# Kernel optimization log

Hardware: AMD Instinct MI355X
Metric: run time of the kernel (lower is better)

The kernel has to match this reference:

```python
import jax, jax.numpy as jnp
import numpy as np

C = 128          # multiplicity of 0e and 1o irreps
N = 16384        # number of tokens / points
SQRT2 = 2.0 ** 0.5
SQRT3 = 3.0 ** 0.5


def _tensor_square(s, v):
    """Per-channel symmetric tensor square of (1x0e + 1x1o).
    s: (N,C) scalars, v: (N,C,3) vectors.
    Returns ss:(N,C) 0e, sv:(N,C,3) 1o, vv0:(N,C) 0e, q:(N,C,5) 2e."""
    ss = s * s
    sv = SQRT2 * s[..., None] * v
    vv0 = jnp.sum(v * v, axis=-1) / SQRT3
    x, y, z = v[..., 0], v[..., 1], v[..., 2]
    q = jnp.stack([
        SQRT3 * x * y,
        SQRT3 * y * z,
        (2.0 * z * z - x * x - y * y) / 2.0,
        SQRT3 * x * z,
        SQRT3 * (x * x - y * y) / 2.0,
    ], axis=-1)
    return ss, sv, vv0, q


def _block(s, v, w1, w2, w0, wv):
    """_SelfInteractionBlock: tensor_square + concat/regroup + invariant-gated MLP + equivariant Linear."""
    ss, sv, vv0, q = _tensor_square(s, v)
    # regrouped features: 3C x 0e, 2C x 1o, C x 2e
    sc = jnp.concatenate([s, ss, vv0], axis=-1)            # (N, 3C)
    vec = jnp.concatenate([v, sv], axis=1)                 # (N, 2C, 3)
    # gate MLP on invariants (fan-in normalized, silu hidden)
    h = jax.nn.silu(sc @ w1 / jnp.sqrt(jnp.float32(sc.shape[-1])))
    g = h @ w2 / jnp.sqrt(jnp.float32(h.shape[-1]))        # (N, 6C) one gate per irrep
    g_s = g[:, :3 * C]
    g_v = g[:, 3 * C:5 * C]
    # (2e gates multiply q, which is dropped by the Linear to Cx0e+Cx1o)
    sc = sc * g_s
    vec = vec * g_v[..., None]
    # block-diagonal equivariant Linear -> C x 0e + C x 1o
    out_s = sc @ w0 / jnp.sqrt(jnp.float32(sc.shape[-1]))                      # (N, C)
    out_v = jnp.einsum('nmd,mc->ncd', vec, wv) / jnp.sqrt(jnp.float32(vec.shape[1]))  # (N, C, 3)
    return out_s, out_v


def _eq_layernorm(s, v, g0, g1, eps=1e-6):
    mu = jnp.mean(s, axis=-1, keepdims=True)
    sd = jnp.sqrt(jnp.mean((s - mu) ** 2, axis=-1, keepdims=True) + eps)
    s = (s - mu) / sd * g0
    rms = jnp.sqrt(jnp.mean(v * v, axis=(1, 2), keepdims=True) + eps)
    v = v / rms * g1[None, :, None]
    return s, v


def setup_inputs() -> dict:
    key = jax.random.key(0)
    ks = jax.random.split(key, 6)
    x = jax.random.normal(ks[0], (N, 4 * C), dtype=jnp.float32)
    mlp_w1 = jax.random.normal(ks[1], (2, 3 * C, 3 * C), dtype=jnp.float32)
    mlp_w2 = jax.random.normal(ks[2], (2, 3 * C, 6 * C), dtype=jnp.float32)
    lin_w0 = jax.random.normal(ks[3], (2, 3 * C, C), dtype=jnp.float32)
    lin_w1 = jax.random.normal(ks[4], (2, 2 * C, C), dtype=jnp.float32)
    ln_g0 = jnp.ones((C,), dtype=jnp.float32)
    ln_g1 = jnp.ones((C,), dtype=jnp.float32)
    return {"x": x, "mlp_w1": mlp_w1, "mlp_w2": mlp_w2,
            "lin_w0": lin_w0, "lin_w1": lin_w1, "ln_g0": ln_g0, "ln_g1": ln_g1}


def reference(x, mlp_w1, mlp_w2, lin_w0, lin_w1, ln_g0, ln_g1):
    n = x.shape[0]
    s = x[:, :C]                         # C x 0e
    v = x[:, C:].reshape(n, C, 3)        # C x 1o
    n_layers = mlp_w1.shape[0]
    for i in range(n_layers):
        ds, dv = _block(s, v, mlp_w1[i], mlp_w2[i], lin_w0[i], lin_w1[i])
        s = s + ds   # residual
        v = v + dv
        if i != n_layers - 1:  # norm on all but last layer (norm_last=False)
            s, v = _eq_layernorm(s, v, ln_g0, ln_g1)
    return jnp.concatenate([s, v.reshape(n, 3 * C)], axis=-1)
```

## Files before the change

kernel.cpp:

```cpp
#include <hip/hip_runtime.h>


typedef _Float16 half8 __attribute__((ext_vector_type(8)));
typedef float floatx4 __attribute__((ext_vector_type(4)));

static inline int cdiv_h(int a, int b){ return (a + b - 1) / b; }


__device__ __forceinline__ void stage16(const char* gaddr, char* lds_base){
  __builtin_amdgcn_global_load_lds((const __attribute__((address_space(1))) unsigned int*)gaddr,
                                   (__attribute__((address_space(3))) unsigned int*)lds_base,
                                   16, 0, 0);
}

__device__ __forceinline__ float wave_sum64(float x){
  #pragma unroll
  for (int m = 32; m; m >>= 1) x += __shfl_xor(x, m, 64);
  return x;
}

__device__ __forceinline__ void split_store(_Float16* p0, _Float16* p1, float v){
  _Float16 hi = (_Float16)v;
  *p0 = hi;
  *p1 = (_Float16)(v - (float)hi);
}

__device__ __forceinline__ unsigned int pack_split(float v){
  union { _Float16 h[2]; unsigned int u; } pk;
  _Float16 hi = (_Float16)v;
  pk.h[0] = hi;
  pk.h[1] = (_Float16)(v - (float)hi);
  return pk.u;
}

__device__ __forceinline__ void unzip16(uint4 p, uint2& hi, uint2& lo){
  hi.x = (p.x & 0xffffu) | (p.y << 16);
  hi.y = (p.z & 0xffffu) | (p.w << 16);
  lo.x = (p.x >> 16) | (p.y & 0xffff0000u);
  lo.y = (p.z >> 16) | (p.w & 0xffff0000u);
}

__device__ __forceinline__ void remap_xcd(int id, int nx, int ny, int& x, int& y){
  if (ny & 7){ x = id % nx; y = id / nx; return; }
  int xcd = id & 7, q = id >> 3, t = q / nx;
  x = q - t*nx; y = xcd + (t << 3);
}

__global__ __launch_bounds__(256) void prep_all(const float* __restrict__ w1,
                                                const float* __restrict__ w2,
                                                const float* __restrict__ w0,
                                                const float* __restrict__ wv,
                                                _Float16* __restrict__ W){
  const int PER_L = 475136;
  int idx = blockIdx.x*256 + threadIdx.x;
  if (idx >= 2*PER_L) return;
  int l = idx / PER_L;
  int r = idx - l*PER_L;
  const float RS384 = 0.051031036307982884f;
  _Float16* WL = W + (size_t)l*1425408;
  const float* src; _Float16* dst; int K, ldw, col, k; float scale;
  if (r < 147456){
    src = w1 + (size_t)l*147456; dst = WL;            K = 384; ldw = 384; scale = RS384;
    col = r / 384; k = r - col*384;
  } else if (r < 393216){
    r -= 147456;
    src = w2 + (size_t)l*294912; dst = WL + 442368;   K = 384; ldw = 768; scale = RS384;
    col = r / 384; k = r - col*384;
  } else if (r < 442368){
    r -= 393216;
    src = w0 + (size_t)l*49152;  dst = WL + 1179648;  K = 384; ldw = 128; scale = RS384;
    col = r / 384; k = r - col*384;
  } else {
    r -= 442368;
    src = wv + (size_t)l*32768;  dst = WL + 1327104;  K = 256; ldw = 128; scale = 0.0625f;
    col = r / 256; k = r - col*256;
  }
  float v = src[(size_t)k*ldw + col] * scale;
  _Float16 hi = (_Float16)v;
  _Float16 lo = (_Float16)(v - (float)hi);
  size_t b = (size_t)col*3*K + k;
  dst[b]       = hi;
  dst[b + K]   = lo;
  dst[b + 2*K] = hi;
}

__global__ __launch_bounds__(256) void e0_fused(const float* __restrict__ x,
                                                float* __restrict__ S,
                                                float* __restrict__ V,
                                                _Float16* __restrict__ A1,
                                                int row0){
  __shared__ alignas(16) float lx[4][512];
  const int n0 = blockIdx.x*4;
  const int tid = threadIdx.x;
  const float4* xs = (const float4*)(x + (size_t)(row0 + n0)*512);
  float4* ls = (float4*)(&lx[0][0]);
  ls[tid]       = xs[tid];
  ls[tid + 256] = xs[tid + 256];
  __syncthreads();
  const int w = tid >> 6, lane = tid & 63;
  const int n = n0 + w;
  const float* row = &lx[w][0];
  #pragma unroll
  for (int h = 0; h < 2; ++h){
    int ch = h*64 + lane;
    float s = row[ch];
    S[(size_t)n*128 + ch] = s;
    float vv = 0.f;
    #pragma unroll
    for (int d = 0; d < 3; ++d){
      float vd = row[128 + ch*3 + d];
      V[((size_t)n*3 + d)*128 + ch] = vd;
      vv += vd*vd;
    }
    float vals[3] = { s, s*s, vv * 0.5773502691896258f };
    #pragma unroll
    for (int q = 0; q < 3; ++q){
      size_t b = (size_t)n*768 + q*128 + ch;
      split_store(&A1[b], &A1[b + 384], vals[q]);
    }
  }
}

__global__ __launch_bounds__(256) void e3_fin(float* __restrict__ S, float* __restrict__ V,
                                              const float* __restrict__ OS, const float* __restrict__ OV,
                                              const float* __restrict__ g0, const float* __restrict__ g1,
                                              float* __restrict__ out, _Float16* __restrict__ A1,
                                              int row0, int doln){
  int n = blockIdx.x*4 + (threadIdx.x >> 6);
  int lane = threadIdx.x & 63;
  size_t sb = (size_t)n*128;
  size_t vb = (size_t)n*384;
  float s0 = S[sb + lane]      + OS[sb + lane];
  float s1 = S[sb + 64 + lane] + OS[sb + 64 + lane];
  float v[6];
  #pragma unroll
  for (int k = 0; k < 6; ++k) v[k] = V[vb + k*64 + lane] + OV[vb + k*64 + lane];

  if (doln){
    float mu = wave_sum64(s0 + s1) * (1.0f/128.0f);
    float d0 = s0 - mu, d1 = s1 - mu;
    float var = wave_sum64(d0*d0 + d1*d1) * (1.0f/128.0f);
    float sd = sqrtf(var + 1e-6f);
    float vvsum = 0.f;
    #pragma unroll
    for (int k = 0; k < 6; ++k) vvsum += v[k]*v[k];
    float rms = sqrtf(wave_sum64(vvsum) * (1.0f/384.0f) + 1e-6f);
    float s0n = d0 / sd * g0[lane];
    float s1n = d1 / sd * g0[64 + lane];
    S[sb + lane]      = s0n;
    S[sb + 64 + lane] = s1n;
    float vn[6];
    #pragma unroll
    for (int k = 0; k < 6; ++k){
      int j = k*64 + lane;
      vn[k] = v[k] / rms * g1[j & 127];
      V[vb + j] = vn[k];
    }
    float vv_a = vn[0]*vn[0] + vn[2]*vn[2] + vn[4]*vn[4];
    float vv_b = vn[1]*vn[1] + vn[3]*vn[3] + vn[5]*vn[5];
    float va[3] = { s0n, s0n*s0n, vv_a * 0.5773502691896258f };
    float vbv[3]= { s1n, s1n*s1n, vv_b * 0.5773502691896258f };
    #pragma unroll
    for (int q = 0; q < 3; ++q){
      size_t ba = (size_t)n*768 + q*128 + lane;
      split_store(&A1[ba], &A1[ba + 384], va[q]);
      size_t bb = ba + 64;
      split_store(&A1[bb], &A1[bb + 384], vbv[q]);
    }
  } else {
    size_t ob = (size_t)(row0 + n)*512;
    out[ob + lane]      = s0;
    out[ob + 64 + lane] = s1;
    #pragma unroll
    for (int k = 0; k < 6; ++k){
      int j = k*64 + lane;
      int d = j >> 7, ch = j & 127;
      out[ob + 128 + ch*3 + d] = v[k];
    }
  }
}

__device__ __forceinline__ void gemm_mainloop(const _Float16* __restrict__ A,
                                              const _Float16* __restrict__ BT,
                                              int lda, int kbase, int m0, int c0,
                                              _Float16 (&lsA)[2][4096],
                                              _Float16 (&lsB)[2][2048],
                                              floatx4 (&acc)[4][2]){
  const int nsc  = kbase >> 5;
  const int nch  = 3*nsc;
  const int ldbt = 3*kbase;
  const int tid  = threadIdx.x;
  const int wave = tid >> 6, lane = tid & 63;
  const int wm = wave & 1, wn = wave >> 1;
  const int r = lane & 15, kg = lane >> 4;
  const int slot = kg ^ ((r >> 1) & 3);

  auto stage = [&](int c, int buf){
    const int ka = ((c < nsc) ? c : c - nsc) << 5;
    const int kb = c << 5;
    #pragma unroll
    for (int p = 0; p < 2; ++p){
      const int lbase = wave*1024 + p*4096;
      const int off = lbase + lane*16;
      const int row = off >> 6;
      const int bir = (off & 63) ^ (((off >> 7) & 3) << 4);
      const char* ga = (const char*)A + (((size_t)(m0 + row))*lda + ka)*2 + bir;
      stage16(ga, (char*)(&lsA[buf][0]) + lbase);
    }
    {
      const int lbase = wave*1024;
      const int off = lbase + lane*16;
      const int row = off >> 6;
      const int bir = (off & 63) ^ (((off >> 7) & 3) << 4);
      const char* gb = (const char*)BT + (((size_t)(c0 + row))*ldbt + kb)*2 + bir;
      stage16(gb, (char*)(&lsB[buf][0]) + lbase);
    }
  };

  stage(0, 0);
  for (int c = 0; c < nch; ++c){
    __syncthreads();
    if (c + 1 < nch) stage(c + 1, (c + 1) & 1);
    const char* a_ = (const char*)&lsA[c & 1][0];
    const char* b_ = (const char*)&lsB[c & 1][0];
    half8 af[4], bf[2];
    #pragma unroll
    for (int mt = 0; mt < 4; ++mt)
      af[mt] = *(const half8*)(a_ + ((wm*64 + mt*16 + r)*64 + slot*16));
    #pragma unroll
    for (int nt = 0; nt < 2; ++nt)
      bf[nt] = *(const half8*)(b_ + ((wn*32 + nt*16 + r)*64 + slot*16));
    #pragma unroll
    for (int mt = 0; mt < 4; ++mt)
      #pragma unroll
      for (int nt = 0; nt < 2; ++nt)
        acc[mt][nt] = __builtin_amdgcn_mfma_f32_16x16x32_f16(af[mt], bf[nt], acc[mt][nt], 0, 0, 0);
  }
}

template<int MODE>
__global__ __launch_bounds__(256, 4) void gemm_split(const _Float16* __restrict__ A,
                                                     const _Float16* __restrict__ BT,
                                                     _Float16* __restrict__ OUT,
                                                     const float* __restrict__ S,
                                                     const float* __restrict__ V,
                                                     _Float16* __restrict__ A1g,
                                                     _Float16* __restrict__ A4,
                                                     int lda, int kbase, int nx, int ny){
  __shared__ alignas(16) _Float16 lsA[2][4096];
  __shared__ alignas(16) _Float16 lsB[2][2048];
  int bx, by; remap_xcd(blockIdx.x, nx, ny, bx, by);
  const int c0 = bx << 6, m0 = by << 7;
  floatx4 acc[4][2];
  #pragma unroll
  for (int i = 0; i < 4; ++i)
    #pragma unroll
    for (int j = 0; j < 2; ++j) acc[i][j] = (floatx4){0.f, 0.f, 0.f, 0.f};

  gemm_mainloop(A, BT, lda, kbase, m0, c0, lsA, lsB, acc);

  const int tid = threadIdx.x;
  const int wave = tid >> 6, lane = tid & 63;
  const int wm = wave & 1, wn = wave >> 1;
  const int r = lane & 15, kg = lane >> 4;
  char* scr = (char*)&lsA[0][0];

  if (MODE == 1){
    #pragma unroll
    for (int h = 0; h < 2; ++h){
      __syncthreads();
      if (wm == h){
        #pragma unroll
        for (int mt = 0; mt < 4; ++mt)
          #pragma unroll
          for (int nt = 0; nt < 2; ++nt)
            #pragma unroll
            for (int i = 0; i < 4; ++i){
              int rl = mt*16 + kg*4 + i;
              int cl = wn*32 + nt*16 + r;
              int pc = cl ^ (kg << 4);
              float g = acc[mt][nt][i];
              float hh = g / (1.0f + __expf(-g));
              *(unsigned int*)(scr + rl*256 + pc*4) = pack_split(hh);
            }
      }
      __syncthreads();
      #pragma unroll 1
      for (int j = 0; j < 4; ++j){
        int lin = j*256 + tid, rl = lin >> 4, seg = lin & 15;
        int cs = seg ^ (((rl >> 2) & 3) << 2);
        uint4 p = *(const uint4*)(scr + rl*256 + cs*16);
        uint2 hi, lo; unzip16(p, hi, lo);
        _Float16* rowp = OUT + (size_t)(m0 + h*64 + rl)*768 + c0 + seg*4;
        *(uint2*)rowp         = hi;
        *(uint2*)(rowp + 384) = lo;
      }
    }
  } else if (c0 < 384){
    #pragma unroll
    for (int h = 0; h < 2; ++h){
      __syncthreads();
      #pragma unroll 1
      for (int j = 0; j < 2; ++j){
        int lin = j*256 + tid, rl = lin >> 3, seg = lin & 7;
        int cs = seg ^ (((rl >> 2) & 3) << 1);
        const _Float16* gp = A1g + (size_t)(m0 + h*64 + rl)*768 + c0 + seg*8;
        *(float4*)(scr + rl*128 + cs*16)        = *(const float4*)gp;
        *(float4*)(scr + 8192 + rl*128 + cs*16) = *(const float4*)(gp + 384);
      }
      __syncthreads();
      if (wm == h){
        #pragma unroll
        for (int mt = 0; mt < 4; ++mt)
          #pragma unroll
          for (int nt = 0; nt < 2; ++nt)
            #pragma unroll
            for (int i = 0; i < 4; ++i){
              int rl = mt*16 + kg*4 + i;
              int cl = wn*32 + nt*16 + r;
              int pc = cl ^ (kg << 4);
              _Float16* phi = (_Float16*)scr + rl*64 + pc;
              _Float16* plo = (_Float16*)(scr + 8192) + rl*64 + pc;
              float sc = (float)*phi + (float)*plo;
              split_store(phi, plo, sc * acc[mt][nt][i]);
            }
      }
      __syncthreads();
      #pragma unroll 1
      for (int j = 0; j < 2; ++j){
        int lin = j*256 + tid, rl = lin >> 3, seg = lin & 7;
        int cs = seg ^ (((rl >> 2) & 3) << 1);
        _Float16* gp = A1g + (size_t)(m0 + h*64 + rl)*768 + c0 + seg*8;
        *(float4*)gp         = *(const float4*)(scr + rl*128 + cs*16);
        *(float4*)(gp + 384) = *(const float4*)(scr + 8192 + rl*128 + cs*16);
      }
    }
  } else {
    const int mm0 = c0 - 384;
    const int ch0 = mm0 & 127;
    if (mm0 >= 128){
      #pragma unroll
      for (int mt = 0; mt < 4; ++mt)
        #pragma unroll
        for (int nt = 0; nt < 2; ++nt)
          #pragma unroll
          for (int i = 0; i < 4; ++i){
            int row = m0 + wm*64 + mt*16 + kg*4 + i;
            int cl  = wn*32 + nt*16 + r;
            acc[mt][nt][i] *= 1.4142135623730951f * S[(size_t)row*128 + ch0 + cl];
          }
    }
    for (int d = 0; d < 3; ++d){
      #pragma unroll
      for (int h = 0; h < 2; ++h){
        __syncthreads();
        #pragma unroll 1
        for (int j = 0; j < 4; ++j){
          int lin = j*256 + tid, rl = lin >> 4, seg = lin & 15;
          int cs = seg ^ (((rl >> 2) & 3) << 2);
          *(float4*)(scr + rl*256 + cs*16) =
            *(const float4*)(V + ((size_t)(m0 + h*64 + rl)*3 + d)*128 + ch0 + seg*4);
        }
        __syncthreads();
        if (wm == h){
          #pragma unroll
          for (int mt = 0; mt < 4; ++mt)
            #pragma unroll
            for (int nt = 0; nt < 2; ++nt)
              #pragma unroll
              for (int i = 0; i < 4; ++i){
                int rl = mt*16 + kg*4 + i;
                int cl = wn*32 + nt*16 + r;
                int pc = cl ^ (kg << 4);
                float* pw = (float*)(scr + rl*256) + pc;
                *(unsigned int*)pw = pack_split(*pw * acc[mt][nt][i]);
              }
        }
        __syncthreads();
        #pragma unroll 1
        for (int j = 0; j < 4; ++j){
          int lin = j*256 + tid, rl = lin >> 4, seg = lin & 15;
          int cs = seg ^ (((rl >> 2) & 3) << 2);
          uint4 p = *(const uint4*)(scr + rl*256 + cs*16);
          uint2 hi, lo; unzip16(p, hi, lo);
          _Float16* rowp = A4 + ((size_t)(m0 + h*64 + rl)*3 + d)*512 + mm0 + seg*4;
          *(uint2*)rowp         = hi;
          *(uint2*)(rowp + 256) = lo;
        }
      }
    }
  }
}

__global__ __launch_bounds__(256, 4) void gemm_pair(const _Float16* __restrict__ Aa,
                                                    const _Float16* __restrict__ Ba,
                                                    float* __restrict__ Ca, int ny0,
                                                    const _Float16* __restrict__ Ab,
                                                    const _Float16* __restrict__ Bb,
                                                    float* __restrict__ Cb, int ny1){
  __shared__ alignas(16) _Float16 lsA[2][4096];
  __shared__ alignas(16) _Float16 lsB[2][2048];
  const _Float16 *A, *BT; float* C; int lda, kbase, bx, by;
  const int id = blockIdx.x;
  if (id < 2*ny0){
    remap_xcd(id, 2, ny0, bx, by);
    A = Aa; BT = Ba; C = Ca; lda = 768; kbase = 384;
  } else {
    remap_xcd(id - 2*ny0, 2, ny1, bx, by);
    A = Ab; BT = Bb; C = Cb; lda = 512; kbase = 256;
  }
  const int c0 = bx << 6, m0 = by << 7;
  floatx4 acc[4][2];
  #pragma unroll
  for (int i = 0; i < 4; ++i)
    #pragma unroll
    for (int j = 0; j < 2; ++j) acc[i][j] = (floatx4){0.f, 0.f, 0.f, 0.f};

  gemm_mainloop(A, BT, lda, kbase, m0, c0, lsA, lsB, acc);

  const int wave = threadIdx.x >> 6, lane = threadIdx.x & 63;
  const int wm = wave & 1, wn = wave >> 1;
  const int r = lane & 15, kg = lane >> 4;
  #pragma unroll
  for (int mt = 0; mt < 4; ++mt)
    #pragma unroll
    for (int nt = 0; nt < 2; ++nt)
      #pragma unroll
      for (int i = 0; i < 4; ++i){
        const int row = m0 + wm*64 + mt*16 + kg*4 + i;
        const int col = c0 + wn*32 + nt*16 + r;
        C[(size_t)row*128 + col] = acc[mt][nt][i];
      }
}


extern "C" void kernel_launch(void* const* d_in, const int* in_sizes, int n_in,
                              void* d_out, int out_size, void* d_ws, size_t ws_size,
                              hipStream_t stream){
  const float* x  = (const float*)d_in[0];
  const float* w1 = (const float*)d_in[1];
  const float* w2 = (const float*)d_in[2];
  const float* w0 = (const float*)d_in[3];
  const float* wv = (const float*)d_in[4];
  const float* g0 = (const float*)d_in[5];
  const float* g1 = (const float*)d_in[6];
  float* out = (float*)d_out;
  const int N = in_sizes[0] / 512;

  const size_t HL = 1425408;
  _Float16* W = (_Float16*)d_ws;
  const size_t wbytes = 2*HL*2;

  int cnum = 128;
  for (int cc = 1; cc <= 128; cc <<= 1){
    size_t need = wbytes + (size_t)(N/cc)*10240;
    if (need <= ws_size){ cnum = cc; break; }
  }
  const int R = N / cnum;
  const int ny = R / 128;

  char* p = (char*)d_ws + wbytes;
  float*    Sst = (float*)p;     p += (size_t)R*512;
  float*    Vst = (float*)p;     p += (size_t)R*1536;
  _Float16* A1  = (_Float16*)p;  p += (size_t)R*1536;
  _Float16* A2  = (_Float16*)p;  p += (size_t)R*1536;
  _Float16* A4  = (_Float16*)p;  p += (size_t)R*3072;
  float*    OS  = (float*)p;     p += (size_t)R*512;
  float*    OV  = (float*)p;     p += (size_t)R*1536;

  prep_all<<<cdiv_h(2*475136,256),256,0,stream>>>(w1, w2, w0, wv, W);

  for (int chk = 0; chk < cnum; ++chk){
    const int row0 = chk*R;
    e0_fused<<<R/4,256,0,stream>>>(x, Sst, Vst, A1, row0);
    for (int l = 0; l < 2; ++l){
      _Float16* W1p = W + (size_t)l*HL;
      _Float16* W2p = W1p + 442368;
      _Float16* W0p = W1p + 1179648;
      _Float16* WVp = W1p + 1327104;
      gemm_split<1><<<6*ny,256,0,stream>>>(A1, W1p, A2,
          nullptr, nullptr, nullptr, nullptr, 768, 384, 6, ny);
      gemm_split<2><<<10*ny,256,0,stream>>>(A2, W2p, nullptr,
          Sst, Vst, A1, A4, 768, 384, 10, ny);
      gemm_pair<<<8*ny,256,0,stream>>>(A1, W0p, OS, ny, A4, WVp, OV, 3*ny);
      e3_fin<<<R/4,256,0,stream>>>(Sst, Vst, OS, OV, g0, g1, out, A1, row0, (l == 0) ? 1 : 0);
    }
  }
}
```

Baseline: 390.5 us.

## Deepen GEMM LDS pipeline to four stages with explicit vmcnt waits

The GEMM mainloop goes from a double-buffered LDS ring to a 4-deep ring that prefetches three chunks ahead. Each step uses explicit s_waitcnt vmcnt counts and a raw s_barrier, so the wait covers only the chunk about to be read instead of draining every outstanding load. The larger LDS footprint lets the epilogues stage the full 128-row tile at once, which removes the two-half loop and its extra barriers. The cost is more LDS per block: launch bounds drop to 3 blocks per CU, so occupancy and latency hiding across blocks may fall.

```diff
diff --git a/kernel.cpp b/kernel.cpp
--- a/kernel.cpp
+++ b/kernel.cpp
@@ -183,8 +183,8 @@
 __device__ __forceinline__ void gemm_mainloop(const _Float16* __restrict__ A,
                                               const _Float16* __restrict__ BT,
                                               int lda, int kbase, int m0, int c0,
-                                              _Float16 (&lsA)[2][4096],
-                                              _Float16 (&lsB)[2][2048],
+                                              _Float16 (&lsA)[4][4096],
+                                              _Float16 (&lsB)[4][2048],
                                               floatx4 (&acc)[4][2]){
   const int nsc  = kbase >> 5;
   const int nch  = 3*nsc;
@@ -217,12 +217,18 @@
     }
   };
 
-  stage(0, 0);
+  stage(0, 0); stage(1, 1); stage(2, 2);
   for (int c = 0; c < nch; ++c){
-    __syncthreads();
-    if (c + 1 < nch) stage(c + 1, (c + 1) & 1);
-    const char* a_ = (const char*)&lsA[c & 1][0];
-    const char* b_ = (const char*)&lsB[c & 1][0];
+    const int rem = nch - 1 - c;
+    __builtin_amdgcn_sched_barrier(0);
+    if (rem >= 2)      asm volatile("s_waitcnt vmcnt(6) lgkmcnt(0)" ::: "memory");
+    else if (rem == 1) asm volatile("s_waitcnt vmcnt(3) lgkmcnt(0)" ::: "memory");
+    else               asm volatile("s_waitcnt vmcnt(0) lgkmcnt(0)" ::: "memory");
+    __builtin_amdgcn_s_barrier();
+    __builtin_amdgcn_sched_barrier(0);
+    if (c + 3 < nch) stage(c + 3, (c + 3) & 3);
+    const char* a_ = (const char*)&lsA[c & 3][0];
+    const char* b_ = (const char*)&lsB[c & 3][0];
     half8 af[4], bf[2];
     #pragma unroll
     for (int mt = 0; mt < 4; ++mt)
@@ -239,7 +245,7 @@
 }
 
 template<int MODE>
-__global__ __launch_bounds__(256, 4) void gemm_split(const _Float16* __restrict__ A,
+__global__ __launch_bounds__(256, 3) void gemm_split(const _Float16* __restrict__ A,
                                                      const _Float16* __restrict__ BT,
                                                      _Float16* __restrict__ OUT,
                                                      const float* __restrict__ S,
@@ -247,8 +253,8 @@
                                                      _Float16* __restrict__ A1g,
                                                      _Float16* __restrict__ A4,
                                                      int lda, int kbase, int nx, int ny){
-  __shared__ alignas(16) _Float16 lsA[2][4096];
-  __shared__ alignas(16) _Float16 lsB[2][2048];
+  __shared__ alignas(16) _Float16 lsA[4][4096];
+  __shared__ alignas(16) _Float16 lsB[4][2048];
   int bx, by; remap_xcd(blockIdx.x, nx, ny, bx, by);
   const int c0 = bx << 6, m0 = by << 7;
   floatx4 acc[4][2];
@@ -266,74 +272,64 @@
   char* scr = (char*)&lsA[0][0];
 
   if (MODE == 1){
-    #pragma unroll
-    for (int h = 0; h < 2; ++h){
-      __syncthreads();
-      if (wm == h){
+    __syncthreads();
+    #pragma unroll
+    for (int mt = 0; mt < 4; ++mt)
+      #pragma unroll
+      for (int nt = 0; nt < 2; ++nt)
         #pragma unroll
-        for (int mt = 0; mt < 4; ++mt)
-          #pragma unroll
-          for (int nt = 0; nt < 2; ++nt)
-            #pragma unroll
-            for (int i = 0; i < 4; ++i){
-              int rl = mt*16 + kg*4 + i;
-              int cl = wn*32 + nt*16 + r;
-              int pc = cl ^ (kg << 4);
-              float g = acc[mt][nt][i];
-              float hh = g / (1.0f + __expf(-g));
-              *(unsigned int*)(scr + rl*256 + pc*4) = pack_split(hh);
-            }
-      }
-      __syncthreads();
-      #pragma unroll 1
-      for (int j = 0; j < 4; ++j){
-        int lin = j*256 + tid, rl = lin >> 4, seg = lin & 15;
-        int cs = seg ^ (((rl >> 2) & 3) << 2);
-        uint4 p = *(const uint4*)(scr + rl*256 + cs*16);
-        uint2 hi, lo; unzip16(p, hi, lo);
-        _Float16* rowp = OUT + (size_t)(m0 + h*64 + rl)*768 + c0 + seg*4;
-        *(uint2*)rowp         = hi;
-        *(uint2*)(rowp + 384) = lo;
-      }
+        for (int i = 0; i < 4; ++i){
+          int rl = wm*64 + mt*16 + kg*4 + i;
+          int cl = wn*32 + nt*16 + r;
+          int pc = cl ^ (kg << 4);
+          float g = acc[mt][nt][i];
+          float hh = g / (1.0f + __expf(-g));
+          *(unsigned int*)(scr + rl*256 + pc*4) = pack_split(hh);
+        }
+    __syncthreads();
+    #pragma unroll 1
+    for (int j = 0; j < 8; ++j){
+      int lin = j*256 + tid, rl = lin >> 4, seg = lin & 15;
+      int cs = seg ^ (((rl >> 2) & 3) << 2);
+      uint4 p = *(const uint4*)(scr + rl*256 + cs*16);
+      uint2 hi, lo; unzip16(p, hi, lo);
+      _Float16* rowp = OUT + (size_t)(m0 + rl)*768 + c0 + seg*4;
+      *(uint2*)rowp         = hi;
+      *(uint2*)(rowp + 384) = lo;
     }
   } else if (c0 < 384){
-    #pragma unroll
-    for (int h = 0; h < 2; ++h){
-      __syncthreads();
-      #pragma unroll 1
-      for (int j = 0; j < 2; ++j){
-        int lin = j*256 + tid, rl = lin >> 3, seg = lin & 7;
-        int cs = seg ^ (((rl >> 2) & 3) << 1);
-        const _Float16* gp = A1g + (size_t)(m0 + h*64 + rl)*768 + c0 + seg*8;
-        *(float4*)(scr + rl*128 + cs*16)        = *(const float4*)gp;
-        *(float4*)(scr + 8192 + rl*128 + cs*16) = *(const float4*)(gp + 384);
-      }
-      __syncthreads();
-      if (wm == h){
+    __syncthreads();
+    #pragma unroll 1
+    for (int j = 0; j < 4; ++j){
+      int lin = j*256 + tid, rl = lin >> 3, seg = lin & 7;
+      int cs = seg ^ (((rl >> 2) & 3) << 1);
+      const _Float16* gp = A1g + (size_t)(m0 + rl)*768 + c0 + seg*8;
+      *(float4*)(scr + rl*128 + cs*16)         = *(const float4*)gp;
+      *(float4*)(scr + 16384 + rl*128 + cs*16) = *(const float4*)(gp + 384);
+    }
+    __syncthreads();
+    #pragma unroll
+    for (int mt = 0; mt < 4; ++mt)
+      #pragma unroll
+      for (int nt = 0; nt < 2; ++nt)
         #pragma unroll
-        for (int mt = 0; mt < 4; ++mt)
-          #pragma unroll
-          for (int nt = 0; nt < 2; ++nt)
-            #pragma unroll
-            for (int i = 0; i < 4; ++i){
-              int rl = mt*16 + kg*4 + i;
-              int cl = wn*32 + nt*16 + r;
-              int pc = cl ^ (kg << 4);
-              _Float16* phi = (_Float16*)scr + rl*64 + pc;
-              _Float16* plo = (_Float16*)(scr + 8192) + rl*64 + pc;
-              float sc = (float)*phi + (float)*plo;
-              split_store(phi, plo, sc * acc[mt][nt][i]);
-            }
-      }
-      __syncthreads();
-      #pragma unroll 1
-      for (int j = 0; j < 2; ++j){
-        int lin = j*256 + tid, rl = lin >> 3, seg = lin & 7;
-        int cs = seg ^ (((rl >> 2) & 3) << 1);
-        _Float16* gp = A1g + (size_t)(m0 + h*64 + rl)*768 + c0 + seg*8;
-        *(float4*)gp         = *(const float4*)(scr + rl*128 + cs*16);
-        *(float4*)(gp + 384) = *(const float4*)(scr + 8192 + rl*128 + cs*16);
-      }
+        for (int i = 0; i < 4; ++i){
+          int rl = wm*64 + mt*16 + kg*4 + i;
+          int cl = wn*32 + nt*16 + r;
+          int pc = cl ^ (kg << 4);
+          _Float16* phi = (_Float16*)scr + rl*64 + pc;
+          _Float16* plo = (_Float16*)(scr + 16384) + rl*64 + pc;
+          float sc = (float)*phi + (float)*plo;
+          split_store(phi, plo, sc * acc[mt][nt][i]);
+        }
+    __syncthreads();
+    #pragma unroll 1
+    for (int j = 0; j < 4; ++j){
+      int lin = j*256 + tid, rl = lin >> 3, seg = lin & 7;
+      int cs = seg ^ (((rl >> 2) & 3) << 1);
+      _Float16* gp = A1g + (size_t)(m0 + rl)*768 + c0 + seg*8;
+      *(float4*)gp         = *(const float4*)(scr + rl*128 + cs*16);
+      *(float4*)(gp + 384) = *(const float4*)(scr + 16384 + rl*128 + cs*16);
     }
   } else {
     const int mm0 = c0 - 384;
@@ -351,55 +347,50 @@
           }
     }
     for (int d = 0; d < 3; ++d){
-      #pragma unroll
-      for (int h = 0; h < 2; ++h){
-        __syncthreads();
-        #pragma unroll 1
-        for (int j = 0; j < 4; ++j){
-          int lin = j*256 + tid, rl = lin >> 4, seg = lin & 15;
-          int cs = seg ^ (((rl >> 2) & 3) << 2);
-          *(float4*)(scr + rl*256 + cs*16) =
-            *(const float4*)(V + ((size_t)(m0 + h*64 + rl)*3 + d)*128 + ch0 + seg*4);
-        }
-        __syncthreads();
-        if (wm == h){
+      __syncthreads();
+      #pragma unroll 1
+      for (int j = 0; j < 8; ++j){
+        int lin = j*256 + tid, rl = lin >> 4, seg = lin & 15;
+        int cs = seg ^ (((rl >> 2) & 3) << 2);
+        *(float4*)(scr + rl*256 + cs*16) =
+          *(const float4*)(V + ((size_t)(m0 + rl)*3 + d)*128 + ch0 + seg*4);
+      }
+      __syncthreads();
+      #pragma unroll
+      for (int mt = 0; mt < 4; ++mt)
+        #pragma unroll
+        for (int nt = 0; nt < 2; ++nt)
           #pragma unroll
-          for (int mt = 0; mt < 4; ++mt)
-            #pragma unroll
-            for (int nt = 0; nt < 2; ++nt)
-              #pragma unroll
-              for (int i = 0; i < 4; ++i){
-                int rl = mt*16 + kg*4 + i;
-                int cl = wn*32 + nt*16 + r;
-                int pc = cl ^ (kg << 4);
-                float* pw = (float*)(scr + rl*256) + pc;
-                *(unsigned int*)pw = pack_split(*pw * acc[mt][nt][i]);
-              }
-        }
-        __syncthreads();
-        #pragma unroll 1
-        for (int j = 0; j < 4; ++j){
-          int lin = j*256 + tid, rl = lin >> 4, seg = lin & 15;
-          int cs = seg ^ (((rl >> 2) & 3) << 2);
-          uint4 p = *(const uint4*)(scr + rl*256 + cs*16);
-          uint2 hi, lo; unzip16(p, hi, lo);
-          _Float16* rowp = A4 + ((size_t)(m0 + h*64 + rl)*3 + d)*512 + mm0 + seg*4;
-          *(uint2*)rowp         = hi;
-          *(uint2*)(rowp + 256) = lo;
-        }
+          for (int i = 0; i < 4; ++i){
+            int rl = wm*64 + mt*16 + kg*4 + i;
+            int cl = wn*32 + nt*16 + r;
+            int pc = cl ^ (kg << 4);
+            float* pw = (float*)(scr + rl*256) + pc;
+            *(unsigned int*)pw = pack_split(*pw * acc[mt][nt][i]);
+          }
+      __syncthreads();
+      #pragma unroll 1
+      for (int j = 0; j < 8; ++j){
+        int lin = j*256 + tid, rl = lin >> 4, seg = lin & 15;
+        int cs = seg ^ (((rl >> 2) & 3) << 2);
+        uint4 p = *(const uint4*)(scr + rl*256 + cs*16);
+        uint2 hi, lo; unzip16(p, hi, lo);
+        _Float16* rowp = A4 + ((size_t)(m0 + rl)*3 + d)*512 + mm0 + seg*4;
+        *(uint2*)rowp         = hi;
+        *(uint2*)(rowp + 256) = lo;
       }
     }
   }
 }
 
-__global__ __launch_bounds__(256, 4) void gemm_pair(const _Float16* __restrict__ Aa,
+__global__ __launch_bounds__(256, 3) void gemm_pair(const _Float16* __restrict__ Aa,
                                                     const _Float16* __restrict__ Ba,
                                                     float* __restrict__ Ca, int ny0,
                                                     const _Float16* __restrict__ Ab,
                                                     const _Float16* __restrict__ Bb,
                                                     float* __restrict__ Cb, int ny1){
-  __shared__ alignas(16) _Float16 lsA[2][4096];
-  __shared__ alignas(16) _Float16 lsB[2][2048];
+  __shared__ alignas(16) _Float16 lsA[4][4096];
+  __shared__ alignas(16) _Float16 lsB[4][2048];
   const _Float16 *A, *BT; float* C; int lda, kbase, bx, by;
   const int id = blockIdx.x;
   if (id < 2*ny0){
```

Result: slower. 412.3 us (+5.6%).

## Widen GEMM block tiles from 128x64 to 128x128 across all split GEMMs

Applied to the files above, without the earlier changes.

Doubles the N-dimension of each GEMM workgroup tile to 128 columns, so each wave computes a 64x64 sub-tile with 16 MFMA accumulators instead of 8. A and B now share one LDS buffer, and all epilogues (silu gating, scalar/vector gating, the A4 scatter) are re-indexed for the wider tile. Grids are halved, which cuts redundant A-tile loads and raises MFMA work per LDS read. The cost is more accumulator registers, which may hurt occupancy under launch_bounds(256,4), and fewer workgroups to fill the GPU.

```diff
diff --git a/kernel.cpp b/kernel.cpp
--- a/kernel.cpp
+++ b/kernel.cpp
@@ -183,9 +183,8 @@
 __device__ __forceinline__ void gemm_mainloop(const _Float16* __restrict__ A,
                                               const _Float16* __restrict__ BT,
                                               int lda, int kbase, int m0, int c0,
-                                              _Float16 (&lsA)[2][4096],
-                                              _Float16 (&lsB)[2][2048],
-                                              floatx4 (&acc)[4][2]){
+                                              _Float16 (&ls)[2][8192],
+                                              floatx4 (&acc)[4][4]){
   const int nsc  = kbase >> 5;
   const int nch  = 3*nsc;
   const int ldbt = 3*kbase;
@@ -205,15 +204,9 @@
       const int row = off >> 6;
       const int bir = (off & 63) ^ (((off >> 7) & 3) << 4);
       const char* ga = (const char*)A + (((size_t)(m0 + row))*lda + ka)*2 + bir;
-      stage16(ga, (char*)(&lsA[buf][0]) + lbase);
-    }
-    {
-      const int lbase = wave*1024;
-      const int off = lbase + lane*16;
-      const int row = off >> 6;
-      const int bir = (off & 63) ^ (((off >> 7) & 3) << 4);
+      stage16(ga, (char*)(&ls[buf][0]) + lbase);
       const char* gb = (const char*)BT + (((size_t)(c0 + row))*ldbt + kb)*2 + bir;
-      stage16(gb, (char*)(&lsB[buf][0]) + lbase);
+      stage16(gb, (char*)(&ls[buf][4096]) + lbase);
     }
   };
 
@@ -221,19 +214,19 @@
   for (int c = 0; c < nch; ++c){
     __syncthreads();
     if (c + 1 < nch) stage(c + 1, (c + 1) & 1);
-    const char* a_ = (const char*)&lsA[c & 1][0];
-    const char* b_ = (const char*)&lsB[c & 1][0];
-    half8 af[4], bf[2];
+    const char* a_ = (const char*)&ls[c & 1][0];
+    const char* b_ = (const char*)&ls[c & 1][4096];
+    half8 af[4], bf[4];
     #pragma unroll
     for (int mt = 0; mt < 4; ++mt)
       af[mt] = *(const half8*)(a_ + ((wm*64 + mt*16 + r)*64 + slot*16));
     #pragma unroll
-    for (int nt = 0; nt < 2; ++nt)
-      bf[nt] = *(const half8*)(b_ + ((wn*32 + nt*16 + r)*64 + slot*16));
+    for (int nt = 0; nt < 4; ++nt)
+      bf[nt] = *(const half8*)(b_ + ((wn*64 + nt*16 + r)*64 + slot*16));
     #pragma unroll
     for (int mt = 0; mt < 4; ++mt)
       #pragma unroll
-      for (int nt = 0; nt < 2; ++nt)
+      for (int nt = 0; nt < 4; ++nt)
         acc[mt][nt] = __builtin_amdgcn_mfma_f32_16x16x32_f16(af[mt], bf[nt], acc[mt][nt], 0, 0, 0);
   }
 }
@@ -247,23 +240,22 @@
                                                      _Float16* __restrict__ A1g,
                                                      _Float16* __restrict__ A4,
                                                      int lda, int kbase, int nx, int ny){
-  __shared__ alignas(16) _Float16 lsA[2][4096];
-  __shared__ alignas(16) _Float16 lsB[2][2048];
+  __shared__ alignas(16) _Float16 ls[2][8192];
   int bx, by; remap_xcd(blockIdx.x, nx, ny, bx, by);
-  const int c0 = bx << 6, m0 = by << 7;
-  floatx4 acc[4][2];
+  const int c0 = bx << 7, m0 = by << 7;
+  floatx4 acc[4][4];
   #pragma unroll
   for (int i = 0; i < 4; ++i)
     #pragma unroll
-    for (int j = 0; j < 2; ++j) acc[i][j] = (floatx4){0.f, 0.f, 0.f, 0.f};
-
-  gemm_mainloop(A, BT, lda, kbase, m0, c0, lsA, lsB, acc);
+    for (int j = 0; j < 4; ++j) acc[i][j] = (floatx4){0.f, 0.f, 0.f, 0.f};
+
+  gemm_mainloop(A, BT, lda, kbase, m0, c0, ls, acc);
 
   const int tid = threadIdx.x;
   const int wave = tid >> 6, lane = tid & 63;
   const int wm = wave & 1, wn = wave >> 1;
   const int r = lane & 15, kg = lane >> 4;
-  char* scr = (char*)&lsA[0][0];
+  char* scr = (char*)&ls[0][0];
 
   if (MODE == 1){
     #pragma unroll
@@ -273,81 +265,80 @@
         #pragma unroll
         for (int mt = 0; mt < 4; ++mt)
           #pragma unroll
-          for (int nt = 0; nt < 2; ++nt)
+          for (int nt = 0; nt < 4; ++nt)
             #pragma unroll
             for (int i = 0; i < 4; ++i){
               int rl = mt*16 + kg*4 + i;
-              int cl = wn*32 + nt*16 + r;
+              int cl = wn*64 + nt*16 + r;
               int pc = cl ^ (kg << 4);
               float g = acc[mt][nt][i];
               float hh = g / (1.0f + __expf(-g));
-              *(unsigned int*)(scr + rl*256 + pc*4) = pack_split(hh);
+              *(unsigned int*)(scr + rl*512 + pc*4) = pack_split(hh);
             }
       }
+      __syncthreads();
+      #pragma unroll 1
+      for (int j = 0; j < 8; ++j){
+        int lin = j*256 + tid, rl = lin >> 5, seg = lin & 31;
+        int cs = seg ^ (((rl >> 2) & 3) << 2);
+        uint4 p = *(const uint4*)(scr + rl*512 + cs*16);
+        uint2 hi, lo; unzip16(p, hi, lo);
+        _Float16* rowp = OUT + (size_t)(m0 + h*64 + rl)*768 + c0 + seg*4;
+        *(uint2*)rowp         = hi;
+        *(uint2*)(rowp + 384) = lo;
+      }
+    }
+  } else if (c0 < 384){
+    #pragma unroll
+    for (int h = 0; h < 2; ++h){
       __syncthreads();
       #pragma unroll 1
       for (int j = 0; j < 4; ++j){
         int lin = j*256 + tid, rl = lin >> 4, seg = lin & 15;
-        int cs = seg ^ (((rl >> 2) & 3) << 2);
-        uint4 p = *(const uint4*)(scr + rl*256 + cs*16);
-        uint2 hi, lo; unzip16(p, hi, lo);
-        _Float16* rowp = OUT + (size_t)(m0 + h*64 + rl)*768 + c0 + seg*4;
-        *(uint2*)rowp         = hi;
-        *(uint2*)(rowp + 384) = lo;
-      }
-    }
-  } else if (c0 < 384){
-    #pragma unroll
-    for (int h = 0; h < 2; ++h){
-      __syncthreads();
-      #pragma unroll 1
-      for (int j = 0; j < 2; ++j){
-        int lin = j*256 + tid, rl = lin >> 3, seg = lin & 7;
         int cs = seg ^ (((rl >> 2) & 3) << 1);
         const _Float16* gp = A1g + (size_t)(m0 + h*64 + rl)*768 + c0 + seg*8;
-        *(float4*)(scr + rl*128 + cs*16)        = *(const float4*)gp;
-        *(float4*)(scr + 8192 + rl*128 + cs*16) = *(const float4*)(gp + 384);
+        *(float4*)(scr + rl*256 + cs*16)         = *(const float4*)gp;
+        *(float4*)(scr + 16384 + rl*256 + cs*16) = *(const float4*)(gp + 384);
       }
       __syncthreads();
       if (wm == h){
         #pragma unroll
         for (int mt = 0; mt < 4; ++mt)
           #pragma unroll
-          for (int nt = 0; nt < 2; ++nt)
+          for (int nt = 0; nt < 4; ++nt)
             #pragma unroll
             for (int i = 0; i < 4; ++i){
               int rl = mt*16 + kg*4 + i;
-              int cl = wn*32 + nt*16 + r;
+              int cl = wn*64 + nt*16 + r;
               int pc = cl ^ (kg << 4);
-              _Float16* phi = (_Float16*)scr + rl*64 + pc;
-              _Float16* plo = (_Float16*)(scr + 8192) + rl*64 + pc;
+              _Float16* phi = (_Float16*)scr + rl*128 + pc;
+              _Float16* plo = (_Float16*)(scr + 16384) + rl*128 + pc;
               float sc = (float)*phi + (float)*plo;
               split_store(phi, plo, sc * acc[mt][nt][i]);
             }
       }
       __syncthreads();
       #pragma unroll 1
-      for (int j = 0; j < 2; ++j){
-        int lin = j*256 + tid, rl = lin >> 3, seg = lin & 7;
+      for (int j = 0; j < 4; ++j){
+        int lin = j*256 + tid, rl = lin >> 4, seg = lin & 15;
         int cs = seg ^ (((rl >> 2) & 3) << 1);
         _Float16* gp = A1g + (size_t)(m0 + h*64 + rl)*768 + c0 + seg*8;
-        *(float4*)gp         = *(const float4*)(scr + rl*128 + cs*16);
-        *(float4*)(gp + 384) = *(const float4*)(scr + 8192 + rl*128 + cs*16);
+        *(float4*)gp         = *(const float4*)(scr + rl*256 + cs*16);
+        *(float4*)(gp + 384) = *(const float4*)(scr + 16384 + rl*256 + cs*16);
       }
     }
   } else {
     const int mm0 = c0 - 384;
-    const int ch0 = mm0 & 127;
-    if (mm0 >= 128){
+    if (mm0 == 128){
       #pragma unroll
       for (int mt = 0; mt < 4; ++mt)
         #pragma unroll
-        for (int nt = 0; nt < 2; ++nt)
+        for (int nt = 0; nt < 4; ++nt)
           #pragma unroll
           for (int i = 0; i < 4; ++i){
             int row = m0 + wm*64 + mt*16 + kg*4 + i;
-            int cl  = wn*32 + nt*16 + r;
-            acc[mt][nt][i] *= 1.4142135623730951f * S[(size_t)row*128 + ch0 + cl];
+            int cl  = wn*64 + nt*16 + r;
+            acc[mt][nt][i] *= 1.4142135623730951f * S[(size_t)row*128 + cl];
           }
     }
     for (int d = 0; d < 3; ++d){
@@ -355,33 +346,33 @@
       for (int h = 0; h < 2; ++h){
         __syncthreads();
         #pragma unroll 1
-        for (int j = 0; j < 4; ++j){
-          int lin = j*256 + tid, rl = lin >> 4, seg = lin & 15;
+        for (int j = 0; j < 8; ++j){
+          int lin = j*256 + tid, rl = lin >> 5, seg = lin & 31;
           int cs = seg ^ (((rl >> 2) & 3) << 2);
-          *(float4*)(scr + rl*256 + cs*16) =
-            *(const float4*)(V + ((size_t)(m0 + h*64 + rl)*3 + d)*128 + ch0 + seg*4);
+          *(float4*)(scr + rl*512 + cs*16) =
+            *(const float4*)(V + ((size_t)(m0 + h*64 + rl)*3 + d)*128 + seg*4);
         }
         __syncthreads();
         if (wm == h){
           #pragma unroll
           for (int mt = 0; mt < 4; ++mt)
             #pragma unroll
-            for (int nt = 0; nt < 2; ++nt)
+            for (int nt = 0; nt < 4; ++nt)
               #pragma unroll
               for (int i = 0; i < 4; ++i){
                 int rl = mt*16 + kg*4 + i;
-                int cl = wn*32 + nt*16 + r;
+                int cl = wn*64 + nt*16 + r;
                 int pc = cl ^ (kg << 4);
-                float* pw = (float*)(scr + rl*256) + pc;
+                float* pw = (float*)(scr + rl*512) + pc;
                 *(unsigned int*)pw = pack_split(*pw * acc[mt][nt][i]);
               }
         }
         __syncthreads();
         #pragma unroll 1
-        for (int j = 0; j < 4; ++j){
-          int lin = j*256 + tid, rl = lin >> 4, seg = lin & 15;
+        for (int j = 0; j < 8; ++j){
+          int lin = j*256 + tid, rl = lin >> 5, seg = lin & 31;
           int cs = seg ^ (((rl >> 2) & 3) << 2);
-          uint4 p = *(const uint4*)(scr + rl*256 + cs*16);
+          uint4 p = *(const uint4*)(scr + rl*512 + cs*16);
           uint2 hi, lo; unzip16(p, hi, lo);
           _Float16* rowp = A4 + ((size_t)(m0 + h*64 + rl)*3 + d)*512 + mm0 + seg*4;
           *(uint2*)rowp         = hi;
@@ -398,25 +389,24 @@
                                                     const _Float16* __restrict__ Ab,
                                                     const _Float16* __restrict__ Bb,
                                                     float* __restrict__ Cb, int ny1){
-  __shared__ alignas(16) _Float16 lsA[2][4096];
-  __shared__ alignas(16) _Float16 lsB[2][2048];
+  __shared__ alignas(16) _Float16 ls[2][8192];
   const _Float16 *A, *BT; float* C; int lda, kbase, bx, by;
   const int id = blockIdx.x;
-  if (id < 2*ny0){
-    remap_xcd(id, 2, ny0, bx, by);
+  if (id < ny0){
+    remap_xcd(id, 1, ny0, bx, by);
     A = Aa; BT = Ba; C = Ca; lda = 768; kbase = 384;
   } else {
-    remap_xcd(id - 2*ny0, 2, ny1, bx, by);
+    remap_xcd(id - ny0, 1, ny1, bx, by);
     A = Ab; BT = Bb; C = Cb; lda = 512; kbase = 256;
   }
-  const int c0 = bx << 6, m0 = by << 7;
-  floatx4 acc[4][2];
+  const int m0 = by << 7;
+  floatx4 acc[4][4];
   #pragma unroll
   for (int i = 0; i < 4; ++i)
     #pragma unroll
-    for (int j = 0; j < 2; ++j) acc[i][j] = (floatx4){0.f, 0.f, 0.f, 0.f};
-
-  gemm_mainloop(A, BT, lda, kbase, m0, c0, lsA, lsB, acc);
+    for (int j = 0; j < 4; ++j) acc[i][j] = (floatx4){0.f, 0.f, 0.f, 0.f};
+
+  gemm_mainloop(A, BT, lda, kbase, m0, 0, ls, acc);
 
   const int wave = threadIdx.x >> 6, lane = threadIdx.x & 63;
   const int wm = wave & 1, wn = wave >> 1;
@@ -424,11 +414,11 @@
   #pragma unroll
   for (int mt = 0; mt < 4; ++mt)
     #pragma unroll
-    for (int nt = 0; nt < 2; ++nt)
+    for (int nt = 0; nt < 4; ++nt)
       #pragma unroll
       for (int i = 0; i < 4; ++i){
         const int row = m0 + wm*64 + mt*16 + kg*4 + i;
-        const int col = c0 + wn*32 + nt*16 + r;
+        const int col = wn*64 + nt*16 + r;
         C[(size_t)row*128 + col] = acc[mt][nt][i];
       }
 }
@@ -478,11 +468,11 @@
       _Float16* W2p = W1p + 442368;
       _Float16* W0p = W1p + 1179648;
       _Float16* WVp = W1p + 1327104;
-      gemm_split<1><<<6*ny,256,0,stream>>>(A1, W1p, A2,
-          nullptr, nullptr, nullptr, nullptr, 768, 384, 6, ny);
-      gemm_split<2><<<10*ny,256,0,stream>>>(A2, W2p, nullptr,
-          Sst, Vst, A1, A4, 768, 384, 10, ny);
-      gemm_pair<<<8*ny,256,0,stream>>>(A1, W0p, OS, ny, A4, WVp, OV, 3*ny);
+      gemm_split<1><<<3*ny,256,0,stream>>>(A1, W1p, A2,
+          nullptr, nullptr, nullptr, nullptr, 768, 384, 3, ny);
+      gemm_split<2><<<5*ny,256,0,stream>>>(A2, W2p, nullptr,
+          Sst, Vst, A1, A4, 768, 384, 5, ny);
+      gemm_pair<<<4*ny,256,0,stream>>>(A1, W0p, OS, ny, A4, WVp, OV, 3*ny);
       e3_fin<<<R/4,256,0,stream>>>(Sst, Vst, OS, OV, g0, g1, out, A1, row0, (l == 0) ? 1 : 0);
     }
   }
```

New measurement: 407.8 us. 1.04x slower.

## Stage hi and lo split-fp16 tiles together and issue three MFMAs per chunk

Applied to the files above, without the earlier changes.

The split-fp16 GEMM previously ran the K loop over a tripled K dimension (hi*hi, lo-part, hi-part concatenated), restaging A and B for each third. Now each K chunk loads A-hi, A-lo, B-hi and B-lo into one enlarged LDS buffer and issues the three cross-product MFMA sets from the same registers. This cuts loop iterations, barriers and redundant reloads of the A hi tile. The weight layout drops the duplicated hi copy. The cost is more LDS per block (48KB versus 24KB), so the occupancy hint drops from 4 to 3 blocks.

```diff
diff --git a/kernel.cpp b/kernel.cpp
--- a/kernel.cpp
+++ b/kernel.cpp
@@ -57,31 +57,30 @@
   int l = idx / PER_L;
   int r = idx - l*PER_L;
   const float RS384 = 0.051031036307982884f;
-  _Float16* WL = W + (size_t)l*1425408;
+  _Float16* WL = W + (size_t)l*950272;
   const float* src; _Float16* dst; int K, ldw, col, k; float scale;
   if (r < 147456){
     src = w1 + (size_t)l*147456; dst = WL;            K = 384; ldw = 384; scale = RS384;
     col = r / 384; k = r - col*384;
   } else if (r < 393216){
     r -= 147456;
-    src = w2 + (size_t)l*294912; dst = WL + 442368;   K = 384; ldw = 768; scale = RS384;
+    src = w2 + (size_t)l*294912; dst = WL + 294912;   K = 384; ldw = 768; scale = RS384;
     col = r / 384; k = r - col*384;
   } else if (r < 442368){
     r -= 393216;
-    src = w0 + (size_t)l*49152;  dst = WL + 1179648;  K = 384; ldw = 128; scale = RS384;
+    src = w0 + (size_t)l*49152;  dst = WL + 786432;   K = 384; ldw = 128; scale = RS384;
     col = r / 384; k = r - col*384;
   } else {
     r -= 442368;
-    src = wv + (size_t)l*32768;  dst = WL + 1327104;  K = 256; ldw = 128; scale = 0.0625f;
+    src = wv + (size_t)l*32768;  dst = WL + 884736;   K = 256; ldw = 128; scale = 0.0625f;
     col = r / 256; k = r - col*256;
   }
   float v = src[(size_t)k*ldw + col] * scale;
   _Float16 hi = (_Float16)v;
   _Float16 lo = (_Float16)(v - (float)hi);
-  size_t b = (size_t)col*3*K + k;
-  dst[b]       = hi;
-  dst[b + K]   = lo;
-  dst[b + 2*K] = hi;
+  size_t b = (size_t)col*2*K + k;
+  dst[b]     = hi;
+  dst[b + K] = lo;
 }
 
 __global__ __launch_bounds__(256) void e0_fused(const float* __restrict__ x,
@@ -183,12 +182,10 @@
 __device__ __forceinline__ void gemm_mainloop(const _Float16* __restrict__ A,
                                               const _Float16* __restrict__ BT,
                                               int lda, int kbase, int m0, int c0,
-                                              _Float16 (&lsA)[2][4096],
-                                              _Float16 (&lsB)[2][2048],
+                                              _Float16 (&ls)[2][12288],
                                               floatx4 (&acc)[4][2]){
   const int nsc  = kbase >> 5;
-  const int nch  = 3*nsc;
-  const int ldbt = 3*kbase;
+  const int ldbt = 2*kbase;
   const int tid  = threadIdx.x;
   const int wave = tid >> 6, lane = tid & 63;
   const int wm = wave & 1, wn = wave >> 1;
@@ -196,50 +193,69 @@
   const int slot = kg ^ ((r >> 1) & 3);
 
   auto stage = [&](int c, int buf){
-    const int ka = ((c < nsc) ? c : c - nsc) << 5;
-    const int kb = c << 5;
+    const int ka = c << 5;
+    char* lb = (char*)(&ls[buf][0]);
     #pragma unroll
     for (int p = 0; p < 2; ++p){
       const int lbase = wave*1024 + p*4096;
       const int off = lbase + lane*16;
       const int row = off >> 6;
       const int bir = (off & 63) ^ (((off >> 7) & 3) << 4);
-      const char* ga = (const char*)A + (((size_t)(m0 + row))*lda + ka)*2 + bir;
-      stage16(ga, (char*)(&lsA[buf][0]) + lbase);
+      const char* gah = (const char*)A + (((size_t)(m0 + row))*lda + ka)*2 + bir;
+      stage16(gah, lb + lbase);
+      const char* gal = (const char*)A + (((size_t)(m0 + row))*lda + kbase + ka)*2 + bir;
+      stage16(gal, lb + 8192 + lbase);
     }
     {
       const int lbase = wave*1024;
       const int off = lbase + lane*16;
       const int row = off >> 6;
       const int bir = (off & 63) ^ (((off >> 7) & 3) << 4);
-      const char* gb = (const char*)BT + (((size_t)(c0 + row))*ldbt + kb)*2 + bir;
-      stage16(gb, (char*)(&lsB[buf][0]) + lbase);
+      const char* gbh = (const char*)BT + (((size_t)(c0 + row))*ldbt + ka)*2 + bir;
+      stage16(gbh, lb + 16384 + lbase);
+      const char* gbl = (const char*)BT + (((size_t)(c0 + row))*ldbt + kbase + ka)*2 + bir;
+      stage16(gbl, lb + 20480 + lbase);
     }
   };
 
   stage(0, 0);
-  for (int c = 0; c < nch; ++c){
+  for (int c = 0; c < nsc; ++c){
     __syncthreads();
-    if (c + 1 < nch) stage(c + 1, (c + 1) & 1);
-    const char* a_ = (const char*)&lsA[c & 1][0];
-    const char* b_ = (const char*)&lsB[c & 1][0];
-    half8 af[4], bf[2];
-    #pragma unroll
-    for (int mt = 0; mt < 4; ++mt)
-      af[mt] = *(const half8*)(a_ + ((wm*64 + mt*16 + r)*64 + slot*16));
-    #pragma unroll
-    for (int nt = 0; nt < 2; ++nt)
-      bf[nt] = *(const half8*)(b_ + ((wn*32 + nt*16 + r)*64 + slot*16));
+    if (c + 1 < nsc) stage(c + 1, (c + 1) & 1);
+    const char* base = (const char*)&ls[c & 1][0];
+    half8 ah[4], al[4], bh[2], bl[2];
+    #pragma unroll
+    for (int mt = 0; mt < 4; ++mt){
+      const int ro = (wm*64 + mt*16 + r)*64 + slot*16;
+      ah[mt] = *(const half8*)(base + ro);
+      al[mt] = *(const half8*)(base + 8192 + ro);
+    }
+    #pragma unroll
+    for (int nt = 0; nt < 2; ++nt){
+      const int ro = (wn*32 + nt*16 + r)*64 + slot*16;
+      bh[nt] = *(const half8*)(base + 16384 + ro);
+      bl[nt] = *(const half8*)(base + 20480 + ro);
+    }
     #pragma unroll
     for (int mt = 0; mt < 4; ++mt)
       #pragma unroll
       for (int nt = 0; nt < 2; ++nt)
-        acc[mt][nt] = __builtin_amdgcn_mfma_f32_16x16x32_f16(af[mt], bf[nt], acc[mt][nt], 0, 0, 0);
+        acc[mt][nt] = __builtin_amdgcn_mfma_f32_16x16x32_f16(ah[mt], bh[nt], acc[mt][nt], 0, 0, 0);
+    #pragma unroll
+    for (int mt = 0; mt < 4; ++mt)
+      #pragma unroll
+      for (int nt = 0; nt < 2; ++nt)
+        acc[mt][nt] = __builtin_amdgcn_mfma_f32_16x16x32_f16(ah[mt], bl[nt], acc[mt][nt], 0, 0, 0);
+    #pragma unroll
+    for (int mt = 0; mt < 4; ++mt)
+      #pragma unroll
+      for (int nt = 0; nt < 2; ++nt)
+        acc[mt][nt] = __builtin_amdgcn_mfma_f32_16x16x32_f16(al[mt], bh[nt], acc[mt][nt], 0, 0, 0);
   }
 }
 
 template<int MODE>
-__global__ __launch_bounds__(256, 4) void gemm_split(const _Float16* __restrict__ A,
+__global__ __launch_bounds__(256, 3) void gemm_split(const _Float16* __restrict__ A,
                                                      const _Float16* __restrict__ BT,
                                                      _Float16* __restrict__ OUT,
                                                      const float* __restrict__ S,
@@ -247,8 +263,7 @@
                                                      _Float16* __restrict__ A1g,
                                                      _Float16* __restrict__ A4,
                                                      int lda, int kbase, int nx, int ny){
-  __shared__ alignas(16) _Float16 lsA[2][4096];
-  __shared__ alignas(16) _Float16 lsB[2][2048];
+  __shared__ alignas(16) _Float16 ls[2][12288];
   int bx, by; remap_xcd(blockIdx.x, nx, ny, bx, by);
   const int c0 = bx << 6, m0 = by << 7;
   floatx4 acc[4][2];
@@ -257,13 +272,13 @@
     #pragma unroll
     for (int j = 0; j < 2; ++j) acc[i][j] = (floatx4){0.f, 0.f, 0.f, 0.f};
 
-  gemm_mainloop(A, BT, lda, kbase, m0, c0, lsA, lsB, acc);
+  gemm_mainloop(A, BT, lda, kbase, m0, c0, ls, acc);
 
   const int tid = threadIdx.x;
   const int wave = tid >> 6, lane = tid & 63;
   const int wm = wave & 1, wn = wave >> 1;
   const int r = lane & 15, kg = lane >> 4;
-  char* scr = (char*)&lsA[0][0];
+  char* scr = (char*)&ls[0][0];
 
   if (MODE == 1){
     #pragma unroll
@@ -392,14 +407,13 @@
   }
 }
 
-__global__ __launch_bounds__(256, 4) void gemm_pair(const _Float16* __restrict__ Aa,
+__global__ __launch_bounds__(256, 3) void gemm_pair(const _Float16* __restrict__ Aa,
                                                     const _Float16* __restrict__ Ba,
                                                     float* __restrict__ Ca, int ny0,
                                                     const _Float16* __restrict__ Ab,
                                                     const _Float16* __restrict__ Bb,
                                                     float* __restrict__ Cb, int ny1){
-  __shared__ alignas(16) _Float16 lsA[2][4096];
-  __shared__ alignas(16) _Float16 lsB[2][2048];
+  __shared__ alignas(16) _Float16 ls[2][12288];
   const _Float16 *A, *BT; float* C; int lda, kbase, bx, by;
   const int id = blockIdx.x;
   if (id < 2*ny0){
@@ -416,7 +430,7 @@
     #pragma unroll
     for (int j = 0; j < 2; ++j) acc[i][j] = (floatx4){0.f, 0.f, 0.f, 0.f};
 
-  gemm_mainloop(A, BT, lda, kbase, m0, c0, lsA, lsB, acc);
+  gemm_mainloop(A, BT, lda, kbase, m0, c0, ls, acc);
 
   const int wave = threadIdx.x >> 6, lane = threadIdx.x & 63;
   const int wm = wave & 1, wn = wave >> 1;
@@ -447,7 +461,7 @@
   float* out = (float*)d_out;
   const int N = in_sizes[0] / 512;
 
-  const size_t HL = 1425408;
+  const size_t HL = 950272;
   _Float16* W = (_Float16*)d_ws;
   const size_t wbytes = 2*HL*2;
 
@@ -475,9 +489,9 @@
     e0_fused<<<R/4,256,0,stream>>>(x, Sst, Vst, A1, row0);
     for (int l = 0; l < 2; ++l){
       _Float16* W1p = W + (size_t)l*HL;
-      _Float16* W2p = W1p + 442368;
-      _Float16* W0p = W1p + 1179648;
-      _Float16* WVp = W1p + 1327104;
+      _Float16* W2p = W1p + 294912;
+      _Float16* W0p = W1p + 786432;
+      _Float16* WVp = W1p + 884736;
       gemm_split<1><<<6*ny,256,0,stream>>>(A1, W1p, A2,
           nullptr, nullptr, nullptr, nullptr, 768, 384, 6, ny);
       gemm_split<2><<<10*ny,256,0,stream>>>(A2, W2p, nullptr,
```

Result: faster. 357.4 us (-8.5%).
